# Kernel tuning notes

Measured on AMD Instinct MI355X. Metric: run time of the kernel, lower is better.

Reference implementation:

```python
import jax, jax.numpy as jnp
import numpy as np

EPS = 1e-12  # matches torch F.normalize default eps


def _l2norm(x):
    # F.normalize(x, dim=-1): x / max(||x||, eps)
    n = jnp.sqrt(jnp.sum(x * x, axis=-1, keepdims=True))
    return x / jnp.maximum(n, EPS)


def setup_inputs() -> dict:
    key = jax.random.key(0)
    kq, kk, kv = jax.random.split(key, 3)
    B, H, N, D = 8, 16, 1024, 64
    q = jax.random.normal(kq, (B, H, N, D), dtype=jnp.float32)
    k = jax.random.normal(kk, (B, H, N, D), dtype=jnp.float32)
    v = jax.random.normal(kv, (B, H, N, D), dtype=jnp.float32)
    return {"q": q, "k": k, "v": v}


def reference(q, k, v):
    B, H, N, D = q.shape
    qn = _l2norm(q)  # [B,H,N,D]
    kn = _l2norm(k)  # [B,H,N,D]
    # cosine-similarity attention logits: [B,H,N,N]
    attn = jnp.einsum("bhnd,bhmd->bhnm", qn, kn)
    attn = jax.nn.softmax(attn, axis=-1)
    # attn_drop is identity (p=0)
    x = jnp.einsum("bhnm,bhmd->bhnd", attn, v)  # [B,H,N,D]
    # transpose(1,2).reshape(B, -1, H*D)
    x = jnp.transpose(x, (0, 2, 1, 3)).reshape(B, N, H * D)
    return x
```

## Files before the change

kernel.cpp:

```cpp
#include <hip/hip_runtime.h>
#include <stdint.h>

typedef __attribute__((ext_vector_type(8))) short short8;
typedef __attribute__((ext_vector_type(4))) float floatx4;

#define B_   8
#define H_   16
#define N_   1024
#define D_   64
#define NH_  (B_*H_)
#define LOG2E 1.44269504088896340736f

#define KS_STRIDE 72
#define VS_STRIDE 68

extern "C" {
__device__ float __ocml_native_exp2_f32(float);
__device__ float __ocml_native_rsqrt_f32(float);
}

__device__ __forceinline__ unsigned int pk2(float a, float b) {
    unsigned int ua = __float_as_uint(a) + 0x8000u;
    unsigned int ub = __float_as_uint(b) + 0x8000u;
    return __builtin_amdgcn_perm(ub, ua, 0x07060302);
}

__global__ __launch_bounds__(256, 2) void attn_fused(
    const float* __restrict__ q, const float* __restrict__ k,
    const float* __restrict__ v, float* __restrict__ out)
{
    __shared__ __align__(16) unsigned short ks[2][64 * KS_STRIDE];
    __shared__ __align__(16) unsigned short vs[2][64 * VS_STRIDE];

    const int bid = blockIdx.x;
    const int xcd = bid & 7, rest = bid >> 3;
    const int qt = rest & 3;
    const int head = (rest >> 2) * 8 + xcd;
    const int tid = threadIdx.x, w = tid >> 6, lane = tid & 63;
    const int lam = lane & 15, quad = lane >> 4;
    const int q0 = qt * 256 + w * 64;

    const float* qh = q + ((size_t)head * N_ + q0) * D_;
    const float* kh = k + (size_t)head * N_ * D_;
    const float* vh = v + (size_t)head * N_ * D_;

    short8 aq[4][2];
    #pragma unroll
    for (int t = 0; t < 4; t++) {
        const float* qr = qh + (t * 16 + lam) * D_ + quad * 8;
        float4 f0 = *(const float4*)(qr);
        float4 f1 = *(const float4*)(qr + 4);
        float4 f2 = *(const float4*)(qr + 32);
        float4 f3 = *(const float4*)(qr + 36);
        float ss = f0.x*f0.x + f0.y*f0.y + f0.z*f0.z + f0.w*f0.w
                 + f1.x*f1.x + f1.y*f1.y + f1.z*f1.z + f1.w*f1.w
                 + f2.x*f2.x + f2.y*f2.y + f2.z*f2.z + f2.w*f2.w
                 + f3.x*f3.x + f3.y*f3.y + f3.z*f3.z + f3.w*f3.w;
        ss += __shfl_xor(ss, 16);
        ss += __shfl_xor(ss, 32);
        float sc = LOG2E * __ocml_native_rsqrt_f32(ss);
        union { unsigned int u[4]; short8 s8; } p0, p1;
        p0.u[0] = pk2(f0.x*sc, f0.y*sc); p0.u[1] = pk2(f0.z*sc, f0.w*sc);
        p0.u[2] = pk2(f1.x*sc, f1.y*sc); p0.u[3] = pk2(f1.z*sc, f1.w*sc);
        p1.u[0] = pk2(f2.x*sc, f2.y*sc); p1.u[1] = pk2(f2.z*sc, f2.w*sc);
        p1.u[2] = pk2(f3.x*sc, f3.y*sc); p1.u[3] = pk2(f3.z*sc, f3.w*sc);
        aq[t][0] = p0.s8; aq[t][1] = p1.s8;
    }

    floatx4 oacc[4][4];
    #pragma unroll
    for (int t = 0; t < 4; t++)
        #pragma unroll
        for (int dt = 0; dt < 4; dt++) oacc[t][dt] = (floatx4){0.f, 0.f, 0.f, 0.f};
    float l[4] = {0.f, 0.f, 0.f, 0.f};

    const int srow = w * 16 + (lane >> 2);
    const int scb  = (lane & 3) * 4;
    const int vswz = ((srow >> 1) & 1) << 1;

    float4 kx[4], vx[4];
    auto gload = [&](int ck) {
        const float* kp = kh + ((size_t)(ck * 64 + srow)) * D_ + scb;
        const float* vp = vh + ((size_t)(ck * 64 + srow)) * D_ + scb;
        #pragma unroll
        for (int i = 0; i < 4; i++) {
            kx[i] = *(const float4*)(kp + 16 * i);
            vx[i] = *(const float4*)(vp + 16 * i);
        }
    };
    auto stage = [&](int buf) {
        float ss = 0.f;
        #pragma unroll
        for (int i = 0; i < 4; i++)
            ss += kx[i].x*kx[i].x + kx[i].y*kx[i].y + kx[i].z*kx[i].z + kx[i].w*kx[i].w;
        ss += __shfl_xor(ss, 1);
        ss += __shfl_xor(ss, 2);
        float sc = __ocml_native_rsqrt_f32(ss);
        #pragma unroll
        for (int i = 0; i < 4; i++) {
            int c = scb + 16 * i;
            unsigned int k0 = pk2(kx[i].x*sc, kx[i].y*sc);
            unsigned int k1 = pk2(kx[i].z*sc, kx[i].w*sc);
            *(uint2*)(&ks[buf][srow * KS_STRIDE + c]) = make_uint2(k0, k1);
            unsigned int v0 = pk2(vx[i].x, vx[i].y);
            unsigned int v1 = pk2(vx[i].z, vx[i].w);
            *(unsigned int*)(&vs[buf][srow * VS_STRIDE + ((c + 0) ^ vswz)]) = v0;
            *(unsigned int*)(&vs[buf][srow * VS_STRIDE + ((c + 2) ^ vswz)]) = v1;
        }
    };

    auto compute = [&](int buf) {
        const unsigned short* ksb = &ks[buf][0];
        const unsigned short* vsb = &vs[buf][0];
        #pragma unroll
        for (int g = 0; g < 2; g++) {
            floatx4 s[4][2];
            #pragma unroll
            for (int s2 = 0; s2 < 2; s2++) {
                int st = g * 2 + s2;
                short8 bk0 = *(const short8*)(ksb + (st * 16 + lam) * KS_STRIDE + quad * 8);
                short8 bk1 = *(const short8*)(ksb + (st * 16 + lam) * KS_STRIDE + 32 + quad * 8);
                #pragma unroll
                for (int t = 0; t < 4; t++) {
                    floatx4 acc = (floatx4){0.f, 0.f, 0.f, 0.f};
                    acc = __builtin_amdgcn_mfma_f32_16x16x32_bf16(bk0, aq[t][0], acc, 0, 0, 0);
                    acc = __builtin_amdgcn_mfma_f32_16x16x32_bf16(bk1, aq[t][1], acc, 0, 0, 0);
                    s[t][s2] = acc;
                }
            }
            short8 pa[4];
            #pragma unroll
            for (int t = 0; t < 4; t++) {
                float e00 = __ocml_native_exp2_f32(s[t][0][0]);
                float e01 = __ocml_native_exp2_f32(s[t][0][1]);
                float e02 = __ocml_native_exp2_f32(s[t][0][2]);
                float e03 = __ocml_native_exp2_f32(s[t][0][3]);
                float e10 = __ocml_native_exp2_f32(s[t][1][0]);
                float e11 = __ocml_native_exp2_f32(s[t][1][1]);
                float e12 = __ocml_native_exp2_f32(s[t][1][2]);
                float e13 = __ocml_native_exp2_f32(s[t][1][3]);
                l[t] += ((e00 + e01) + (e02 + e03)) + ((e10 + e11) + (e12 + e13));
                union { unsigned int u[4]; short8 s8; } pk;
                pk.u[0] = pk2(e00, e01); pk.u[1] = pk2(e02, e03);
                pk.u[2] = pk2(e10, e11); pk.u[3] = pk2(e12, e13);
                pa[t] = pk.s8;
            }
            #pragma unroll
            for (int dt = 0; dt < 4; dt++) {
                union { unsigned short h[8]; short8 s8; } bv;
                #pragma unroll
                for (int j = 0; j < 8; j++) {
                    int key = g * 32 + ((j >> 2) << 4) + quad * 4 + (j & 3);
                    int dsw = ((j >> 1) & 1) << 1;
                    bv.h[j] = vsb[key * VS_STRIDE + ((dt * 16 + lam) ^ dsw)];
                }
                #pragma unroll
                for (int t = 0; t < 4; t++)
                    oacc[t][dt] = __builtin_amdgcn_mfma_f32_16x16x32_bf16(pa[t], bv.s8, oacc[t][dt], 0, 0, 0);
            }
        }
    };

    gload(0);
    stage(0);
    __syncthreads();
    for (int c = 0; c < 16; ++c) {
        int buf = c & 1;
        if (c < 15) gload(c + 1);
        compute(buf);
        if (c < 15) stage(buf ^ 1);
        __syncthreads();
    }

    const int b = head >> 4, hh = head & 15;
    #pragma unroll
    for (int t = 0; t < 4; t++) {
        float lr = l[t];
        lr += __shfl_xor(lr, 16);
        lr += __shfl_xor(lr, 32);
        float rl = 1.0f / lr;
        float rq[4];
        #pragma unroll
        for (int r = 0; r < 4; r++) rq[r] = __shfl(rl, quad * 4 + r);
        float* ob = out + ((size_t)b * N_ + q0 + t * 16) * (H_ * D_) + hh * 64;
        #pragma unroll
        for (int dt = 0; dt < 4; dt++)
            #pragma unroll
            for (int r = 0; r < 4; r++)
                ob[(quad * 4 + r) * (H_ * D_) + dt * 16 + lam] = oacc[t][dt][r] * rq[r];
    }
}

extern "C" void kernel_launch(void* const* d_in, const int* in_sizes, int n_in,
                              void* d_out, int out_size, void* d_ws, size_t ws_size,
                              hipStream_t stream) {
    const float* q = (const float*)d_in[0];
    const float* k = (const float*)d_in[1];
    const float* v = (const float*)d_in[2];
    float* out = (float*)d_out;
    (void)d_ws; (void)ws_size;
    hipLaunchKernelGGL(attn_fused, dim3(NH_ * 4), dim3(256), 0, stream, q, k, v, out);
}
```

Measured before the change: 167.7 us.

## Store V transposed in LDS with XOR swizzle for vectorized B-operand reads

V is now staged transposed in shared memory (d-major, keys contiguous) with an XOR chunk swizzle, and K uses an unpadded 64-wide layout with the same swizzle. The PV MFMA B operand becomes a single 16-byte LDS read instead of eight scalar 2-byte reads, and padding is dropped. To build the transposed layout, each thread loads V from global one scalar at a time across rows, which gives less coalesced global access and more load instructions in exchange for cheaper LDS traffic in the inner loop.

```diff
diff --git a/kernel.cpp b/kernel.cpp
--- a/kernel.cpp
+++ b/kernel.cpp
@@ -11,9 +11,6 @@
 #define NH_  (B_*H_)
 #define LOG2E 1.44269504088896340736f
 
-#define KS_STRIDE 72
-#define VS_STRIDE 68
-
 extern "C" {
 __device__ float __ocml_native_exp2_f32(float);
 __device__ float __ocml_native_rsqrt_f32(float);
@@ -29,8 +26,8 @@
     const float* __restrict__ q, const float* __restrict__ k,
     const float* __restrict__ v, float* __restrict__ out)
 {
-    __shared__ __align__(16) unsigned short ks[2][64 * KS_STRIDE];
-    __shared__ __align__(16) unsigned short vs[2][64 * VS_STRIDE];
+    __shared__ __align__(16) unsigned short ks[2][64 * 64];
+    __shared__ __align__(16) unsigned short vt[2][64 * 64];
 
     const int bid = blockIdx.x;
     const int xcd = bid & 7, rest = bid >> 3;
@@ -38,6 +35,7 @@
     const int head = (rest >> 2) * 8 + xcd;
     const int tid = threadIdx.x, w = tid >> 6, lane = tid & 63;
     const int lam = lane & 15, quad = lane >> 4;
+    const int sw = lam & 7;
     const int q0 = qt * 256 + w * 64;
 
     const float* qh = q + ((size_t)head * N_ + q0) * D_;
@@ -75,51 +73,69 @@
     float l[4] = {0.f, 0.f, 0.f, 0.f};
 
     const int srow = w * 16 + (lane >> 2);
-    const int scb  = (lane & 3) * 4;
-    const int vswz = ((srow >> 1) & 1) << 1;
-
-    float4 kx[4], vx[4];
+    const int kd   = (lane & 3) * 8;
+    const int ksw  = srow & 7;
+    const int vsw  = lane & 7;
+    const int cb0  = 2 * w;
+
+    float4 kx[4];
+    float  vr[2][8];
+
     auto gload = [&](int ck) {
-        const float* kp = kh + ((size_t)(ck * 64 + srow)) * D_ + scb;
-        const float* vp = vh + ((size_t)(ck * 64 + srow)) * D_ + scb;
-        #pragma unroll
-        for (int i = 0; i < 4; i++) {
-            kx[i] = *(const float4*)(kp + 16 * i);
-            vx[i] = *(const float4*)(vp + 16 * i);
+        const float* kp = kh + ((size_t)(ck * 64 + srow)) * D_ + kd;
+        kx[0] = *(const float4*)(kp);
+        kx[1] = *(const float4*)(kp + 4);
+        kx[2] = *(const float4*)(kp + 32);
+        kx[3] = *(const float4*)(kp + 36);
+        #pragma unroll
+        for (int cbi = 0; cbi < 2; cbi++) {
+            int cb = cb0 + cbi;
+            int Lb = ((cb >> 2) << 5) + ((cb & 3) << 2);
+            #pragma unroll
+            for (int j = 0; j < 8; j++) {
+                int L = Lb + ((j >> 2) << 4) + (j & 3);
+                vr[cbi][j] = vh[((size_t)(ck * 64 + L)) * D_ + lane];
+            }
         }
     };
+
     auto stage = [&](int buf) {
-        float ss = 0.f;
-        #pragma unroll
-        for (int i = 0; i < 4; i++)
-            ss += kx[i].x*kx[i].x + kx[i].y*kx[i].y + kx[i].z*kx[i].z + kx[i].w*kx[i].w;
+        float ss = kx[0].x*kx[0].x + kx[0].y*kx[0].y + kx[0].z*kx[0].z + kx[0].w*kx[0].w
+                 + kx[1].x*kx[1].x + kx[1].y*kx[1].y + kx[1].z*kx[1].z + kx[1].w*kx[1].w
+                 + kx[2].x*kx[2].x + kx[2].y*kx[2].y + kx[2].z*kx[2].z + kx[2].w*kx[2].w
+                 + kx[3].x*kx[3].x + kx[3].y*kx[3].y + kx[3].z*kx[3].z + kx[3].w*kx[3].w;
         ss += __shfl_xor(ss, 1);
         ss += __shfl_xor(ss, 2);
         float sc = __ocml_native_rsqrt_f32(ss);
         #pragma unroll
-        for (int i = 0; i < 4; i++) {
-            int c = scb + 16 * i;
-            unsigned int k0 = pk2(kx[i].x*sc, kx[i].y*sc);
-            unsigned int k1 = pk2(kx[i].z*sc, kx[i].w*sc);
-            *(uint2*)(&ks[buf][srow * KS_STRIDE + c]) = make_uint2(k0, k1);
-            unsigned int v0 = pk2(vx[i].x, vx[i].y);
-            unsigned int v1 = pk2(vx[i].z, vx[i].w);
-            *(unsigned int*)(&vs[buf][srow * VS_STRIDE + ((c + 0) ^ vswz)]) = v0;
-            *(unsigned int*)(&vs[buf][srow * VS_STRIDE + ((c + 2) ^ vswz)]) = v1;
+        for (int i = 0; i < 2; i++) {
+            float4 a = kx[2 * i], b = kx[2 * i + 1];
+            union { unsigned int u[4]; short8 s8; } pk;
+            pk.u[0] = pk2(a.x*sc, a.y*sc); pk.u[1] = pk2(a.z*sc, a.w*sc);
+            pk.u[2] = pk2(b.x*sc, b.y*sc); pk.u[3] = pk2(b.z*sc, b.w*sc);
+            int cbk = (lane & 3) + 4 * i;
+            *(short8*)&ks[buf][srow * 64 + ((cbk ^ ksw) << 3)] = pk.s8;
+        }
+        #pragma unroll
+        for (int cbi = 0; cbi < 2; cbi++) {
+            union { unsigned int u[4]; short8 s8; } pv;
+            pv.u[0] = pk2(vr[cbi][0], vr[cbi][1]); pv.u[1] = pk2(vr[cbi][2], vr[cbi][3]);
+            pv.u[2] = pk2(vr[cbi][4], vr[cbi][5]); pv.u[3] = pk2(vr[cbi][6], vr[cbi][7]);
+            *(short8*)&vt[buf][lane * 64 + (((cb0 + cbi) ^ vsw) << 3)] = pv.s8;
         }
     };
 
     auto compute = [&](int buf) {
         const unsigned short* ksb = &ks[buf][0];
-        const unsigned short* vsb = &vs[buf][0];
+        const unsigned short* vsb = &vt[buf][0];
         #pragma unroll
         for (int g = 0; g < 2; g++) {
             floatx4 s[4][2];
             #pragma unroll
             for (int s2 = 0; s2 < 2; s2++) {
                 int st = g * 2 + s2;
-                short8 bk0 = *(const short8*)(ksb + (st * 16 + lam) * KS_STRIDE + quad * 8);
-                short8 bk1 = *(const short8*)(ksb + (st * 16 + lam) * KS_STRIDE + 32 + quad * 8);
+                short8 bk0 = *(const short8*)(ksb + (st * 16 + lam) * 64 + (((0 + quad) ^ sw) << 3));
+                short8 bk1 = *(const short8*)(ksb + (st * 16 + lam) * 64 + (((4 + quad) ^ sw) << 3));
                 #pragma unroll
                 for (int t = 0; t < 4; t++) {
                     floatx4 acc = (floatx4){0.f, 0.f, 0.f, 0.f};
@@ -147,16 +163,10 @@
             }
             #pragma unroll
             for (int dt = 0; dt < 4; dt++) {
-                union { unsigned short h[8]; short8 s8; } bv;
-                #pragma unroll
-                for (int j = 0; j < 8; j++) {
-                    int key = g * 32 + ((j >> 2) << 4) + quad * 4 + (j & 3);
-                    int dsw = ((j >> 1) & 1) << 1;
-                    bv.h[j] = vsb[key * VS_STRIDE + ((dt * 16 + lam) ^ dsw)];
-                }
+                short8 bv = *(const short8*)(vsb + (dt * 16 + lam) * 64 + (((g * 4 + quad) ^ sw) << 3));
                 #pragma unroll
                 for (int t = 0; t < 4; t++)
-                    oacc[t][dt] = __builtin_amdgcn_mfma_f32_16x16x32_bf16(pa[t], bv.s8, oacc[t][dt], 0, 0, 0);
+                    oacc[t][dt] = __builtin_amdgcn_mfma_f32_16x16x32_bf16(pa[t], bv, oacc[t][dt], 0, 0, 0);
             }
         }
     };
```

Measured after the change: 164.5 us. About the same (-1.9%).
